# Optimization experiments

Measured on AMD Instinct MI355X. Metric: run time of the kernel, lower is better.

## Reference

```python
import jax, jax.numpy as jnp
import numpy as np

C = 512
B, H, W = 8, 64, 64
GROUPS = 32
EPS = 1e-6


def setup_inputs() -> dict:
    key = jax.random.key(0)
    ks = jax.random.split(key, 6)
    s = 1.0 / np.sqrt(C)
    return {
        "x": jax.random.normal(ks[0], (B, C, H, W), dtype=jnp.float32),
        "gn_scale": jnp.ones((C,), jnp.float32),
        "gn_bias": jnp.zeros((C,), jnp.float32),
        "wq": jax.random.normal(ks[1], (C, C), jnp.float32) * s,
        "bq": jnp.zeros((C,), jnp.float32),
        "wk": jax.random.normal(ks[2], (C, C), jnp.float32) * s,
        "bk": jnp.zeros((C,), jnp.float32),
        "wv": jax.random.normal(ks[3], (C, C), jnp.float32) * s,
        "bv": jnp.zeros((C,), jnp.float32),
        "wo": jax.random.normal(ks[4], (C, C), jnp.float32) * s,
        "bo": jnp.zeros((C,), jnp.float32),
    }


def group_norm(x, scale, bias):
    # x: [b, c, h, w]; GroupNorm(32 groups, eps=1e-6, affine)
    b, c, h, w = x.shape
    xg = x.reshape(b, GROUPS, c // GROUPS, h, w)
    mean = xg.mean(axis=(2, 3, 4), keepdims=True)
    var = xg.var(axis=(2, 3, 4), keepdims=True)
    xg = (xg - mean) * jax.lax.rsqrt(var + EPS)
    return xg.reshape(b, c, h, w) * scale[None, :, None, None] + bias[None, :, None, None]


def reference(x, gn_scale, gn_bias, wq, bq, wk, bk, wv, bv, wo, bo):
    b, c, h, w = x.shape
    n = h * w
    hn = group_norm(x, gn_scale, gn_bias).reshape(b, c, n)  # [b,c,n]
    # 1x1 convs == channel matmuls
    q = jnp.einsum('oc,bcn->bon', wq, hn) + bq[None, :, None]
    k = jnp.einsum('oc,bcn->bon', wk, hn) + bk[None, :, None]
    v = jnp.einsum('oc,bcn->bon', wv, hn) + bv[None, :, None]
    # scores: [b, n_query, n_key], softmax over keys
    scores = jnp.einsum('bcn,bcm->bnm', q, k) * (float(c) ** -0.5)
    attn = jax.nn.softmax(scores, axis=2)
    # out[b,c,i] = sum_j v[b,c,j] * attn[b,i,j]
    out = jnp.einsum('bcm,bnm->bcn', v, attn)
    out = jnp.einsum('oc,bcn->bon', wo, out) + bo[None, :, None]
    return x + out.reshape(b, c, h, w)
```

## Files before the change

### kernel.cpp

```cpp
#include <hip/hip_runtime.h>
#include <hip/hip_bf16.h>


typedef __bf16 bf16_t;
typedef __bf16 bf16x8 __attribute__((ext_vector_type(8)));
typedef __bf16 bf16x4 __attribute__((ext_vector_type(4)));
typedef float  f32x4  __attribute__((ext_vector_type(4)));

#define CDIM 512
#define NSP  4096
#define L2E  1.4426950408889634f

typedef __attribute__((address_space(1))) const void* as1_cvp;
typedef __attribute__((address_space(3))) void*       as3_vp;

__device__ __forceinline__ void gload_lds16(const void* g, void* l) {
  __builtin_amdgcn_global_load_lds((as1_cvp)g, (as3_vp)l, 16, 0, 0);
}

__global__ __launch_bounds__(256) void f32_to_bf16_k(const float* __restrict__ in,
                                                     bf16_t* __restrict__ out, int n) {
  int i = (blockIdx.x * 256 + threadIdx.x) * 4;
  if (i < n) {
    float4 v = *(const float4*)(in + i);
    bf16x4 o;
    o[0] = (bf16_t)v.x; o[1] = (bf16_t)v.y; o[2] = (bf16_t)v.z; o[3] = (bf16_t)v.w;
    *(bf16x4*)(out + i) = o;
  }
}

__global__ __launch_bounds__(256) void gn_stats_k(const float* __restrict__ x,
                                                  float* __restrict__ stats) {
  const int gid = blockIdx.x;
  const float4* base = (const float4*)(x + (long)gid * 65536);
  float s = 0.f, ss = 0.f;
  for (int i = threadIdx.x; i < 16384; i += 256) {
    float4 t = base[i];
    s  += t.x + t.y + t.z + t.w;
    ss += t.x*t.x + t.y*t.y + t.z*t.z + t.w*t.w;
  }
#pragma unroll
  for (int o = 32; o; o >>= 1) { s += __shfl_xor(s, o); ss += __shfl_xor(ss, o); }
  __shared__ float rs[4], rss[4];
  const int lane = threadIdx.x & 63, wid = threadIdx.x >> 6;
  if (lane == 0) { rs[wid] = s; rss[wid] = ss; }
  __syncthreads();
  if (threadIdx.x == 0) {
    s  = rs[0] + rs[1] + rs[2] + rs[3];
    ss = rss[0] + rss[1] + rss[2] + rss[3];
    float mean = s * (1.f / 65536.f);
    float var  = ss * (1.f / 65536.f) - mean * mean;
    stats[gid]       = mean;
    stats[256 + gid] = rsqrtf(var + 1e-6f);
  }
}

__global__ __launch_bounds__(256) void gn_apply_k(const float* __restrict__ x,
                                                  const float* __restrict__ stats,
                                                  const float* __restrict__ gw,
                                                  const float* __restrict__ gb,
                                                  bf16_t* __restrict__ hnT) {
  __shared__ float tile[64 * 65];
  const int n0 = blockIdx.x * 64;
  const int c0 = blockIdx.y * 64;
  const int b  = blockIdx.z;
  const int tid = threadIdx.x;
  {
    const int cl = tid >> 2, nq = tid & 3;
    const int c = c0 + cl;
    const int g = c >> 4;
    const float mean = stats[b * 32 + g];
    const float rstd = stats[256 + b * 32 + g];
    const float a  = rstd * gw[c];
    const float bb = gb[c] - mean * a;
    const float4* xr = (const float4*)(x + ((long)b * CDIM + c) * NSP + n0 + nq * 16);
#pragma unroll
    for (int i = 0; i < 4; i++) {
      float4 t = xr[i];
      float* d = &tile[cl * 65 + nq * 16 + i * 4];
      d[0] = t.x * a + bb; d[1] = t.y * a + bb; d[2] = t.z * a + bb; d[3] = t.w * a + bb;
    }
  }
  __syncthreads();
  {
    const int nl = tid >> 2, cq = tid & 3;
    union { bf16_t h[16]; uint4 v[2]; } o;
#pragma unroll
    for (int j = 0; j < 16; j++) o.h[j] = (bf16_t)tile[(cq * 16 + j) * 65 + nl];
    bf16_t* dst = hnT + ((long)b * NSP + n0 + nl) * CDIM + c0 + cq * 16;
    ((uint4*)dst)[0] = o.v[0];
    ((uint4*)dst)[1] = o.v[1];
  }
}

template <int MODE>
__global__ __launch_bounds__(256) void gemm_bt_k(
    const bf16_t* __restrict__ A, long sAb, long ldA,
    const bf16_t* __restrict__ B, long sBb, long ldB,
    void* __restrict__ Cout, long sCb, long ldC, void* __restrict__ Cout2,
    int M, int N, int K,
    const float* __restrict__ bias_row,
    const float* __restrict__ bias_col,
    float scale,
    const float* __restrict__ residual, long sRb) {
  __shared__ __align__(16) bf16_t sA[128 * 32];
  __shared__ __align__(16) bf16_t sB[128 * 32];

  const int tid  = threadIdx.x;
  const int lane = tid & 63;
  const int wid  = tid >> 6;
  const int wm = wid >> 1, wn = wid & 1;
  const int b = blockIdx.z;
  const int rowBase = blockIdx.y * 128;
  const int colBase = blockIdx.x * 128;

  const bf16_t* Ab = A + (long)b * sAb + (long)rowBase * ldA;
  const bf16_t* Bb = B + (long)b * sBb + (long)colBase * ldB;

  f32x4 acc[4][4];
#pragma unroll
  for (int i = 0; i < 4; i++)
#pragma unroll
    for (int j = 0; j < 4; j++) acc[i][j] = (f32x4){0.f, 0.f, 0.f, 0.f};

  const int q0 = tid, q1 = tid + 256;
  const int r0 = q0 >> 2, k0c = (q0 & 3) * 8;
  const int r1 = q1 >> 2, k1c = (q1 & 3) * 8;
  const int mrow  = lane & 15;
  const int kfrag = (lane >> 4) * 8;

  for (int kt = 0; kt < K; kt += 32) {
    gload_lds16(Ab + (long)r0 * ldA + kt + k0c, sA + q0 * 8);
    gload_lds16(Ab + (long)r1 * ldA + kt + k1c, sA + q1 * 8);
    gload_lds16(Bb + (long)r0 * ldB + kt + k0c, sB + q0 * 8);
    gload_lds16(Bb + (long)r1 * ldB + kt + k1c, sB + q1 * 8);
    __syncthreads();
    bf16x8 af[4], bfr[4];
#pragma unroll
    for (int t = 0; t < 4; t++) {
      af[t]  = *(const bf16x8*)&sA[(wm * 64 + t * 16 + mrow) * 32 + kfrag];
      bfr[t] = *(const bf16x8*)&sB[(wn * 64 + t * 16 + mrow) * 32 + kfrag];
    }
#pragma unroll
    for (int i = 0; i < 4; i++)
#pragma unroll
      for (int j = 0; j < 4; j++)
        acc[i][j] = __builtin_amdgcn_mfma_f32_16x16x32_bf16(af[i], bfr[j], acc[i][j], 0, 0, 0);
    __syncthreads();
  }

  const int quad = lane >> 4;
  const int colf = lane & 15;
#pragma unroll
  for (int i = 0; i < 4; i++) {
#pragma unroll
    for (int j = 0; j < 4; j++) {
#pragma unroll
      for (int r = 0; r < 4; r++) {
        const int row = rowBase + wm * 64 + i * 16 + quad * 4 + r;
        const int col = colBase + wn * 64 + j * 16 + colf;
        float v = acc[i][j][r];
        if (MODE == 2) {
          if (col < 512)
            ((bf16_t*)Cout)[(long)b * sCb + (long)row * ldC + col] =
                (bf16_t)((v + bias_col[col]) * scale);
          else
            ((bf16_t*)Cout2)[(long)b * sCb + (long)row * ldC + (col - 512)] =
                (bf16_t)(v + bias_row[col - 512]);
        } else {
          if (bias_row) v += bias_row[row];
          if (bias_col) v += bias_col[col];
          v *= scale;
          if (residual) v += residual[(long)b * sRb + (long)row * ldC + col];
          if (MODE == 1)
            ((bf16_t*)Cout)[(long)b * sCb + (long)row * ldC + col] = (bf16_t)v;
          else
            ((float*)Cout)[(long)b * sCb + (long)row * ldC + col] = v;
        }
      }
    }
  }
}

__global__ __launch_bounds__(256, 2) void flash_attn_k(
    const bf16_t* __restrict__ QT, const bf16_t* __restrict__ KT,
    const bf16_t* __restrict__ V, bf16_t* __restrict__ O1T) {
  __shared__ __align__(16) bf16_t sK[64 * 520];
  __shared__ __align__(16) bf16_t sP[4][16 * 72];

  const int tid = threadIdx.x, lane = tid & 63, w = tid >> 6;
  const int quad = lane >> 4, l15 = lane & 15;
  const int b = blockIdx.y, q0 = blockIdx.x * 64;

  const bf16_t* Qw = QT + ((long)b * NSP + q0 + w * 16) * CDIM;
  const bf16_t* Kb = KT + (long)b * NSP * CDIM;
  const bf16_t* Vb = V  + (long)b * NSP * CDIM;

  bf16x8 qf[16];
#pragma unroll
  for (int kc = 0; kc < 16; kc++)
    qf[kc] = *(const bf16x8*)(Qw + (long)l15 * CDIM + kc * 32 + quad * 8);

  f32x4 oacc[32];
#pragma unroll
  for (int i = 0; i < 32; i++) oacc[i] = (f32x4){0.f, 0.f, 0.f, 0.f};
  float m_r[4] = {-3e38f, -3e38f, -3e38f, -3e38f};
  float l_r[4] = {0.f, 0.f, 0.f, 0.f};

  for (int j0 = 0; j0 < NSP; j0 += 64) {
    __syncthreads();
#pragma unroll
    for (int i = 0; i < 16; i++) {
      const int key = w * 16 + i;
      gload_lds16(Kb + (long)(j0 + key) * CDIM + lane * 8, sK + key * 520 + lane * 8);
    }
    __syncthreads();

    f32x4 sacc[4];
#pragma unroll
    for (int t = 0; t < 4; t++) sacc[t] = (f32x4){0.f, 0.f, 0.f, 0.f};
#pragma unroll
    for (int kc = 0; kc < 16; kc++) {
#pragma unroll
      for (int t = 0; t < 4; t++) {
        bf16x8 kf = *(const bf16x8*)(sK + (t * 16 + l15) * 520 + kc * 32 + quad * 8);
        sacc[t] = __builtin_amdgcn_mfma_f32_16x16x32_bf16(qf[kc], kf, sacc[t], 0, 0, 0);
      }
    }

    float alpha[4];
#pragma unroll
    for (int r = 0; r < 4; r++) {
      float mx = fmaxf(fmaxf(sacc[0][r], sacc[1][r]), fmaxf(sacc[2][r], sacc[3][r]));
      mx = fmaxf(mx, __shfl_xor(mx, 1));
      mx = fmaxf(mx, __shfl_xor(mx, 2));
      mx = fmaxf(mx, __shfl_xor(mx, 4));
      mx = fmaxf(mx, __shfl_xor(mx, 8));
      const float mn = fmaxf(m_r[r], mx);
      alpha[r] = exp2f((m_r[r] - mn) * L2E);
      m_r[r] = mn;
      float rs = 0.f;
#pragma unroll
      for (int t = 0; t < 4; t++) {
        const float p = exp2f((sacc[t][r] - mn) * L2E);
        sacc[t][r] = p;
        rs += p;
      }
      rs += __shfl_xor(rs, 1); rs += __shfl_xor(rs, 2);
      rs += __shfl_xor(rs, 4); rs += __shfl_xor(rs, 8);
      l_r[r] = l_r[r] * alpha[r] + rs;
    }
    const f32x4 av = {alpha[0], alpha[1], alpha[2], alpha[3]};
#pragma unroll
    for (int i = 0; i < 32; i++) oacc[i] *= av;

#pragma unroll
    for (int t = 0; t < 4; t++)
#pragma unroll
      for (int r = 0; r < 4; r++)
        sP[w][(quad * 4 + r) * 72 + t * 16 + l15] = (bf16_t)sacc[t][r];
    const bf16x8 pf0 = *(const bf16x8*)(&sP[w][l15 * 72 + quad * 8]);
    const bf16x8 pf1 = *(const bf16x8*)(&sP[w][l15 * 72 + 32 + quad * 8]);

#pragma unroll
    for (int h = 0; h < 2; h++) {
      __syncthreads();
      uint4 tv[8];
#pragma unroll
      for (int i = 0; i < 8; i++) {
        const int g = i * 256 + tid, c = g >> 3, off = g & 7;
        tv[i] = *(const uint4*)(Vb + (long)(h * 256 + c) * NSP + j0 + off * 8);
      }
#pragma unroll
      for (int i = 0; i < 8; i++) {
        const int g = i * 256 + tid, c = g >> 3, off = g & 7;
        *(uint4*)(sK + c * 72 + off * 8) = tv[i];
      }
      __syncthreads();
#pragma unroll
      for (int ct = 0; ct < 16; ct++) {
        const bf16x8 vf0 = *(const bf16x8*)(sK + (ct * 16 + l15) * 72 + quad * 8);
        const bf16x8 vf1 = *(const bf16x8*)(sK + (ct * 16 + l15) * 72 + 32 + quad * 8);
        oacc[h * 16 + ct] =
            __builtin_amdgcn_mfma_f32_16x16x32_bf16(pf0, vf0, oacc[h * 16 + ct], 0, 0, 0);
        oacc[h * 16 + ct] =
            __builtin_amdgcn_mfma_f32_16x16x32_bf16(pf1, vf1, oacc[h * 16 + ct], 0, 0, 0);
      }
    }
  }

  const f32x4 linv = {1.f / l_r[0], 1.f / l_r[1], 1.f / l_r[2], 1.f / l_r[3]};
  __syncthreads();
#pragma unroll
  for (int ct = 0; ct < 32; ct++) {
    const f32x4 o = oacc[ct] * linv;
#pragma unroll
    for (int r = 0; r < 4; r++)
      sK[(w * 16 + quad * 4 + r) * 520 + ct * 16 + l15] = (bf16_t)o[r];
  }
  __syncthreads();
  bf16_t* Ob = O1T + ((long)b * NSP + q0) * CDIM;
#pragma unroll
  for (int i = 0; i < 16; i++) {
    const int g = i * 256 + tid, row = g >> 6, off = g & 63;
    *(uint4*)(Ob + (long)row * CDIM + off * 8) = *(const uint4*)(sK + row * 520 + off * 8);
  }
}

extern "C" void kernel_launch(void* const* d_in, const int* in_sizes, int n_in,
                              void* d_out, int out_size, void* d_ws, size_t ws_size,
                              hipStream_t stream) {
  const float* x        = (const float*)d_in[0];
  const float* gn_scale = (const float*)d_in[1];
  const float* gn_bias  = (const float*)d_in[2];
  const float* wq = (const float*)d_in[3];
  const float* bq = (const float*)d_in[4];
  const float* wk = (const float*)d_in[5];
  const float* bk = (const float*)d_in[6];
  const float* wv = (const float*)d_in[7];
  const float* bv = (const float*)d_in[8];
  const float* wo = (const float*)d_in[9];
  const float* bo = (const float*)d_in[10];
  float* out = (float*)d_out;

  const long PB = 2097152;
  const long MB = 1048576L;
  char* w = (char*)d_ws;
  bf16_t* hnT  = (bf16_t*)(w);
  bf16_t* O1T  = hnT;
  bf16_t* QT   = (bf16_t*)(w + 32 * MB);
  bf16_t* KT   = (bf16_t*)(w + 64 * MB);
  bf16_t* V    = (bf16_t*)(w + 96 * MB);
  bf16_t* wqkb = (bf16_t*)(w + 128 * MB);
  bf16_t* wvb  = (bf16_t*)(w + 129 * MB);
  bf16_t* wob  = (bf16_t*)(w + 129 * MB + 524288L);
  float*  stats = (float*)(w + 130 * MB);

  const float qscale = 0.044194173824159216f;

  f32_to_bf16_k<<<256, 256, 0, stream>>>(wq, wqkb, 262144);
  f32_to_bf16_k<<<256, 256, 0, stream>>>(wk, wqkb + 262144, 262144);
  f32_to_bf16_k<<<256, 256, 0, stream>>>(wv, wvb, 262144);
  f32_to_bf16_k<<<256, 256, 0, stream>>>(wo, wob, 262144);

  gn_stats_k<<<256, 256, 0, stream>>>(x, stats);
  gn_apply_k<<<dim3(64, 8, 8), 256, 0, stream>>>(x, stats, gn_scale, gn_bias, hnT);

  gemm_bt_k<2><<<dim3(8, 32, 8), 256, 0, stream>>>(
      hnT, PB, 512, wqkb, 0, 512, QT, PB, 512, KT, 4096, 1024, 512,
      bk, bq, qscale, nullptr, 0);
  gemm_bt_k<1><<<dim3(32, 4, 8), 256, 0, stream>>>(
      wvb, 0, 512, hnT, PB, 512, V, PB, 4096, nullptr, 512, 4096, 512,
      bv, nullptr, 1.f, nullptr, 0);

  flash_attn_k<<<dim3(64, 8), 256, 0, stream>>>(QT, KT, V, O1T);

  gemm_bt_k<0><<<dim3(32, 4, 8), 256, 0, stream>>>(
      wob, 0, 512, O1T, PB, 512, (void*)out, PB, 4096, nullptr, 512, 4096, 512,
      bo, nullptr, 1.f, x, PB);
}
```

Before: 1.150 ms.

## Halve key tile, load K and V together via swizzled async LDS copies

Shrinks the flash-attention key block from 64 to 32 keys so K and V tiles fit in one shared buffer. Both are loaded with direct global-to-LDS copies, which removes the two extra barrier-separated V staging passes through registers, and XOR swizzling replaces row padding to avoid bank conflicts. It also skips rescaling the output accumulator when no row max changed. The cost is twice as many loop iterations and barriers, and smaller MFMA batches per iteration. The epilogue now reuses the unpadded 512-stride buffer.

```diff
diff --git a/kernel.cpp b/kernel.cpp
--- a/kernel.cpp
+++ b/kernel.cpp
@@ -185,8 +185,10 @@
 __global__ __launch_bounds__(256, 2) void flash_attn_k(
     const bf16_t* __restrict__ QT, const bf16_t* __restrict__ KT,
     const bf16_t* __restrict__ V, bf16_t* __restrict__ O1T) {
-  __shared__ __align__(16) bf16_t sK[64 * 520];
-  __shared__ __align__(16) bf16_t sP[4][16 * 72];
+  __shared__ __align__(16) bf16_t sKV[32 * 512 + 512 * 32];
+  __shared__ __align__(16) bf16_t sP[4][16 * 40];
+  bf16_t* sK = sKV;
+  bf16_t* sV = sKV + 32 * 512;
 
   const int tid = threadIdx.x, lane = tid & 63, w = tid >> 6;
   const int quad = lane >> 4, l15 = lane & 15;
@@ -207,23 +209,37 @@
   float m_r[4] = {-3e38f, -3e38f, -3e38f, -3e38f};
   float l_r[4] = {0.f, 0.f, 0.f, 0.f};
 
-  for (int j0 = 0; j0 < NSP; j0 += 64) {
+  const int kswz = lane ^ 7;
+  (void)kswz;
+
+  for (int j0 = 0; j0 < NSP; j0 += 32) {
     __syncthreads();
-#pragma unroll
-    for (int i = 0; i < 16; i++) {
-      const int key = w * 16 + i;
-      gload_lds16(Kb + (long)(j0 + key) * CDIM + lane * 8, sK + key * 520 + lane * 8);
+
+#pragma unroll
+    for (int i = 0; i < 8; i++) {
+      const int key = w * 8 + i;
+      const int ol = lane ^ (key & 7);
+      gload_lds16(Kb + (long)(j0 + key) * CDIM + ol * 8, sK + key * 512 + lane * 8);
+    }
+#pragma unroll
+    for (int j = 0; j < 8; j++) {
+      const int cbase = w * 128 + j * 16;
+      const int c = cbase + (lane >> 2);
+      const int ol = (lane & 3) ^ (c & 3);
+      gload_lds16(Vb + (long)c * NSP + j0 + ol * 8, sV + cbase * 32 + lane * 8);
     }
     __syncthreads();
 
-    f32x4 sacc[4];
-#pragma unroll
-    for (int t = 0; t < 4; t++) sacc[t] = (f32x4){0.f, 0.f, 0.f, 0.f};
+    f32x4 sacc[2];
+    sacc[0] = (f32x4){0.f, 0.f, 0.f, 0.f};
+    sacc[1] = (f32x4){0.f, 0.f, 0.f, 0.f};
 #pragma unroll
     for (int kc = 0; kc < 16; kc++) {
 #pragma unroll
-      for (int t = 0; t < 4; t++) {
-        bf16x8 kf = *(const bf16x8*)(sK + (t * 16 + l15) * 520 + kc * 32 + quad * 8);
+      for (int t = 0; t < 2; t++) {
+        const int key = t * 16 + l15;
+        const int ch = (kc * 4 + quad) ^ (l15 & 7);
+        bf16x8 kf = *(const bf16x8*)(sK + key * 512 + ch * 8);
         sacc[t] = __builtin_amdgcn_mfma_f32_16x16x32_bf16(qf[kc], kf, sacc[t], 0, 0, 0);
       }
     }
@@ -231,7 +247,7 @@
     float alpha[4];
 #pragma unroll
     for (int r = 0; r < 4; r++) {
-      float mx = fmaxf(fmaxf(sacc[0][r], sacc[1][r]), fmaxf(sacc[2][r], sacc[3][r]));
+      float mx = fmaxf(sacc[0][r], sacc[1][r]);
       mx = fmaxf(mx, __shfl_xor(mx, 1));
       mx = fmaxf(mx, __shfl_xor(mx, 2));
       mx = fmaxf(mx, __shfl_xor(mx, 4));
@@ -241,7 +257,7 @@
       m_r[r] = mn;
       float rs = 0.f;
 #pragma unroll
-      for (int t = 0; t < 4; t++) {
+      for (int t = 0; t < 2; t++) {
         const float p = exp2f((sacc[t][r] - mn) * L2E);
         sacc[t][r] = p;
         rs += p;
@@ -250,42 +266,26 @@
       rs += __shfl_xor(rs, 4); rs += __shfl_xor(rs, 8);
       l_r[r] = l_r[r] * alpha[r] + rs;
     }
-    const f32x4 av = {alpha[0], alpha[1], alpha[2], alpha[3]};
-#pragma unroll
-    for (int i = 0; i < 32; i++) oacc[i] *= av;
-
-#pragma unroll
-    for (int t = 0; t < 4; t++)
+    const float aprod = alpha[0] * alpha[1] * alpha[2] * alpha[3];
+    if (__any(aprod != 1.0f)) {
+      const f32x4 av = {alpha[0], alpha[1], alpha[2], alpha[3]};
+#pragma unroll
+      for (int i = 0; i < 32; i++) oacc[i] *= av;
+    }
+
+#pragma unroll
+    for (int t = 0; t < 2; t++)
 #pragma unroll
       for (int r = 0; r < 4; r++)
-        sP[w][(quad * 4 + r) * 72 + t * 16 + l15] = (bf16_t)sacc[t][r];
-    const bf16x8 pf0 = *(const bf16x8*)(&sP[w][l15 * 72 + quad * 8]);
-    const bf16x8 pf1 = *(const bf16x8*)(&sP[w][l15 * 72 + 32 + quad * 8]);
-
-#pragma unroll
-    for (int h = 0; h < 2; h++) {
-      __syncthreads();
-      uint4 tv[8];
-#pragma unroll
-      for (int i = 0; i < 8; i++) {
-        const int g = i * 256 + tid, c = g >> 3, off = g & 7;
-        tv[i] = *(const uint4*)(Vb + (long)(h * 256 + c) * NSP + j0 + off * 8);
-      }
-#pragma unroll
-      for (int i = 0; i < 8; i++) {
-        const int g = i * 256 + tid, c = g >> 3, off = g & 7;
-        *(uint4*)(sK + c * 72 + off * 8) = tv[i];
-      }
-      __syncthreads();
-#pragma unroll
-      for (int ct = 0; ct < 16; ct++) {
-        const bf16x8 vf0 = *(const bf16x8*)(sK + (ct * 16 + l15) * 72 + quad * 8);
-        const bf16x8 vf1 = *(const bf16x8*)(sK + (ct * 16 + l15) * 72 + 32 + quad * 8);
-        oacc[h * 16 + ct] =
-            __builtin_amdgcn_mfma_f32_16x16x32_bf16(pf0, vf0, oacc[h * 16 + ct], 0, 0, 0);
-        oacc[h * 16 + ct] =
-            __builtin_amdgcn_mfma_f32_16x16x32_bf16(pf1, vf1, oacc[h * 16 + ct], 0, 0, 0);
-      }
+        sP[w][(quad * 4 + r) * 40 + t * 16 + l15] = (bf16_t)sacc[t][r];
+    const bf16x8 pf = *(const bf16x8*)(&sP[w][l15 * 40 + quad * 8]);
+
+#pragma unroll
+    for (int ct = 0; ct < 32; ct++) {
+      const int c = ct * 16 + l15;
+      const int ch = quad ^ (l15 & 3);
+      const bf16x8 vf = *(const bf16x8*)(sV + c * 32 + ch * 8);
+      oacc[ct] = __builtin_amdgcn_mfma_f32_16x16x32_bf16(pf, vf, oacc[ct], 0, 0, 0);
     }
   }
 
@@ -296,14 +296,14 @@
     const f32x4 o = oacc[ct] * linv;
 #pragma unroll
     for (int r = 0; r < 4; r++)
-      sK[(w * 16 + quad * 4 + r) * 520 + ct * 16 + l15] = (bf16_t)o[r];
+      sKV[(w * 16 + quad * 4 + r) * 512 + ct * 16 + l15] = (bf16_t)o[r];
   }
   __syncthreads();
   bf16_t* Ob = O1T + ((long)b * NSP + q0) * CDIM;
 #pragma unroll
   for (int i = 0; i < 16; i++) {
     const int g = i * 256 + tid, row = g >> 6, off = g & 63;
-    *(uint4*)(Ob + (long)row * CDIM + off * 8) = *(const uint4*)(sK + row * 520 + off * 8);
+    *(uint4*)(Ob + (long)row * CDIM + off * 8) = *(const uint4*)(sKV + row * 512 + off * 8);
   }
 }
 
```

New measurement: 1.534 ms. 1.33x slower.
